# Kernel tuning notes

Measured on AMD Instinct MI355X. Metric: run time of the kernel, lower is better.

The kernel has to match this reference:

```python
import jax, jax.numpy as jnp
import numpy as np

B, P, N = 4, 1024, 16
C1, C2 = 64, 64
K, A = 13, 12  # kernel points (12 s2 dirs + center), rotation anchors
EPS = 1e-12


def _icosahedron_vertices():
    phi = (1.0 + 5.0 ** 0.5) / 2.0
    vs = np.array([
        [-1, phi, 0], [1, phi, 0], [-1, -phi, 0], [1, -phi, 0],
        [0, -1, phi], [0, 1, phi], [0, -1, -phi], [0, 1, -phi],
        [phi, 0, -1], [phi, 0, 1], [-phi, 0, -1], [-phi, 0, 1]], dtype=np.float32)
    return vs


def setup_inputs() -> dict:
    key = jax.random.key(0)
    k1, k2, k3, k4, k5, k6, k7 = jax.random.split(key, 7)
    neighbor_index = jax.random.randint(k1, (B, P, N), 0, P, dtype=jnp.int64) if jax.config.jax_enable_x64 else jax.random.randint(k1, (B, P, N), 0, P, dtype=jnp.int32)
    vertices = jax.random.normal(k2, (B, P, 3), dtype=jnp.float32)
    feature_map = jax.random.normal(k3, (B, C1, P, A), dtype=jnp.float32)
    # xavier-normal init for W (dim_out, dim_in, 36)
    std = (2.0 / (C1 * 36 + C2 * 36)) ** 0.5
    W = jax.random.normal(k4, (C2, C1, 36), dtype=jnp.float32) * std
    vs = jnp.asarray(_icosahedron_vertices())
    # structurally-identical index tables (original precomputed from icosahedral symmetry)
    idx_map = jax.random.randint(k5, (K * A,), 0, 36)  # 156 -> 36 shared weights
    trace_idxv_rot = jax.random.randint(k6, (A, K), 0, K)  # per-anchor kernel permutation
    trace_idxv_rot = trace_idxv_rot.at[:, -1].set(K - 1)  # center maps to itself
    trace_idx_rot = jax.random.randint(k7, (A, A), 0, A)  # per-anchor anchor permutation
    return {"neighbor_index": neighbor_index, "vertices": vertices, "feature_map": feature_map,
            "W": W, "vs": vs, "idx_map": idx_map,
            "trace_idxv_rot": trace_idxv_rot, "trace_idx_rot": trace_idx_rot}


def reference(neighbor_index, vertices, feature_map, W, vs, idx_map, trace_idxv_rot, trace_idx_rot):
    b, p, n = neighbor_index.shape
    c2, c1, _ = W.shape
    # neighbor direction (normalized): [b,p,n,3]
    neighbors = jax.vmap(lambda v, idx: v[idx])(vertices, neighbor_index)
    direction = neighbors - vertices[:, :, None, :]
    dn = direction / jnp.maximum(jnp.linalg.norm(direction, axis=-1, keepdims=True), EPS)
    vs_norm = vs / jnp.maximum(jnp.linalg.norm(vs, axis=1, keepdims=True), EPS)
    # correlation of each neighbor direction with the 12 icosahedron dirs: [b,12,p,n]
    vs_theta = jnp.einsum('bpnc,ac->bapn', dn, vs_norm)
    inter_w = jax.nn.softmax(vs_theta, axis=-1)  # softmax over neighbors
    # gather neighbor features: [b,c1,p,n,a]
    feature_neighbor = jax.vmap(lambda f, idx: f[:, idx, :])(feature_map, neighbor_index)
    # soft-assign neighbors to the 12 kernel directions: [b,c1,12,p,a]
    new_feat = jnp.einsum('bkpn,bcpna->bckpa', inter_w, feature_neighbor)
    # append the center kernel point: [b,c1,13,p,a]
    new_feat = jnp.concatenate([new_feat, feature_map[:, :, None]], axis=2)
    # expand shared weights: [c2,c1,13,12]
    Wmap = W[:, :, idx_map].reshape(c2, c1, K, A)
    # rotated weights per output anchor r: W_eff[c2,c1,r,k,a] = Wmap[c2,c1, kk[r,k], aa[r,a]]
    W_eff = Wmap[:, :, trace_idxv_rot[:, :, None], trace_idx_rot[:, None, :]]
    out = jnp.einsum('bckpa,dcrka->bdpr', new_feat, W_eff)  # [b,c2,p,12]
    return out
```

## Files before the change

kernel.cpp:

```cpp
#include <hip/hip_runtime.h>
#include <hip/hip_bf16.h>
#include <hip/hip_fp16.h>

typedef __attribute__((ext_vector_type(8))) short short8;
typedef __attribute__((ext_vector_type(4))) short s16x4;
typedef __attribute__((ext_vector_type(4))) float f32x4;

#define BN 4
#define PN 1024
#define NN 16
#define C1N 64
#define C2N 64
#define KN 13
#define AN 12
#define KDIM 9984
#define NDIM 768
#define MDIM 4096
#define NSPLIT 5
#define BK 64
#define BM 256
#define BNT 256

__device__ inline unsigned short f2bf(float x){
    unsigned int u = __float_as_uint(x);
    unsigned int r = (u + 0x7fffu + ((u >> 16) & 1u)) >> 16;
    return (unsigned short)r;
}
__device__ inline f32x4 bf4_to_f(s16x4 h){
    f32x4 r;
    r[0] = __uint_as_float(((unsigned)(unsigned short)h[0]) << 16);
    r[1] = __uint_as_float(((unsigned)(unsigned short)h[1]) << 16);
    r[2] = __uint_as_float(((unsigned)(unsigned short)h[2]) << 16);
    r[3] = __uint_as_float(((unsigned)(unsigned short)h[3]) << 16);
    return r;
}

__device__ __forceinline__ void gload16(const unsigned short* g, unsigned short* l){
    __builtin_amdgcn_global_load_lds(
        (const __attribute__((address_space(1))) unsigned int*)(unsigned long long)(uintptr_t)g,
        (__attribute__((address_space(3))) unsigned int*)(unsigned int)(uintptr_t)l,
        16, 0, 0);
}

__global__ __launch_bounds__(256) void k_prep(const int* __restrict__ nbr,
                                              const float* __restrict__ vert,
                                              const float* __restrict__ vs,
                                              const float* __restrict__ W,
                                              const int* __restrict__ idx_map,
                                              const int* __restrict__ tiv,
                                              const int* __restrict__ tir,
                                              const float* __restrict__ fm,
                                              float* __restrict__ iw,
                                              unsigned short* __restrict__ Bm,
                                              unsigned short* __restrict__ Am)
{
    int bid = blockIdx.x;
    if (bid < 192){
        int t = bid * 256 + threadIdx.x;
        int pt = t / AN, a = t - pt * AN;
        int b = pt >> 10;
        float sx = vs[a*3+0], sy = vs[a*3+1], sz = vs[a*3+2];
        float sn = sqrtf(sx*sx + sy*sy + sz*sz);
        float si = 1.0f / fmaxf(sn, 1e-12f);
        sx *= si; sy *= si; sz *= si;
        float vx = vert[pt*3+0], vy = vert[pt*3+1], vz = vert[pt*3+2];
        float tt[NN];
        float mx = -1e30f;
        #pragma unroll
        for (int n = 0; n < NN; n++){
            int g = (b << 10) + nbr[pt*NN + n];
            float dx = vert[g*3+0] - vx;
            float dy = vert[g*3+1] - vy;
            float dz = vert[g*3+2] - vz;
            float nr = sqrtf(dx*dx + dy*dy + dz*dz);
            float inv = 1.0f / fmaxf(nr, 1e-12f);
            tt[n] = (dx*sx + dy*sy + dz*sz) * inv;
            mx = fmaxf(mx, tt[n]);
        }
        float s = 0.0f;
        #pragma unroll
        for (int n = 0; n < NN; n++){ tt[n] = expf(tt[n] - mx); s += tt[n]; }
        float inv = 1.0f / s;
        float* dst = iw + (size_t)t * NN;
        #pragma unroll
        for (int q = 0; q < 4; q++){
            float4 v = make_float4(tt[q*4]*inv, tt[q*4+1]*inv, tt[q*4+2]*inv, tt[q*4+3]*inv);
            *(float4*)(dst + q*4) = v;
        }
    } else if (bid < 2688){
        int t = (bid - 192) * 256 + threadIdx.x;
        int c = t & 63;
        int rest = t >> 6;
        int k = rest % KN;
        int rest2 = rest / KN;
        int r = rest2 % AN;
        int d = rest2 / AN;
        int tv = tiv[r*KN + k];
        const float* wrow = W + (size_t)((d << 6) + c) * 36;
        s16x4 v0, v1, v2;
        #pragma unroll
        for (int a = 0; a < AN; a++){
            int s = idx_map[tv*AN + tir[r*AN + a]];
            unsigned short h = f2bf(wrow[s]);
            if (a < 4) v0[a] = (short)h;
            else if (a < 8) v1[a-4] = (short)h;
            else v2[a-8] = (short)h;
        }
        unsigned short* dst = Bm + ((size_t)(d*AN + r) * KDIM + k*768 + c*AN);
        s16x4* d4 = (s16x4*)dst;
        d4[0] = v0; d4[1] = v1; d4[2] = v2;
    } else {
        int t = (bid - 2688) * 256 + threadIdx.x;
        int a4 = t % 3;
        int rest = t / 3;
        int p = rest & 1023;
        int bc = rest >> 10;
        int c = bc & 63, b = bc >> 6;
        float4 v = *(const float4*)(fm + (size_t)rest * 12 + a4*4);
        s16x4 h;
        h[0] = (short)f2bf(v.x); h[1] = (short)f2bf(v.y);
        h[2] = (short)f2bf(v.z); h[3] = (short)f2bf(v.w);
        int m = (b << 10) + p;
        *(s16x4*)(Am + (size_t)m * KDIM + 9216 + c*12 + a4*4) = h;
    }
}

__global__ __launch_bounds__(256) void k_newfeat(const int* __restrict__ nbr,
                                                 const float* __restrict__ iw,
                                                 unsigned short* Am)
{
    __shared__ int   nbs_s[2][NN];
    __shared__ float iwT_s[2][NN][AN];
    int t = threadIdx.x;
    int w = t >> 6, lane = t & 63;
    int pw = w >> 1, khalf = w & 1;
    int m = blockIdx.x * 2 + pw;
    int b = m >> 10;

    if (khalf == 0){
        if (lane < NN) nbs_s[pw][lane] = nbr[m*NN + lane];
        #pragma unroll
        for (int i = 0; i < 3; i++){
            int idx = lane + i*64;
            int a = idx >> 4, n = idx & 15;
            iwT_s[pw][n][a] = iw[(size_t)m * (AN*NN) + idx];
        }
    }
    __syncthreads();

    f32x4 acc[6][3];
    #pragma unroll
    for (int k = 0; k < 6; k++)
        #pragma unroll
        for (int q = 0; q < 3; q++) acc[k][q] = (f32x4){0.f,0.f,0.f,0.f};

    int kb = khalf * 6;
    const unsigned short* slice = Am + 9216 + (size_t)lane * AN;

    #pragma unroll 2
    for (int n = 0; n < NN; n++){
        int mn = (b << 10) + nbs_s[pw][n];
        const unsigned short* src = slice + (size_t)mn * KDIM;
        s16x4 u0 = *(const s16x4*)(src);
        s16x4 u1 = *(const s16x4*)(src + 4);
        s16x4 u2 = *(const s16x4*)(src + 8);
        f32x4 v0 = bf4_to_f(u0), v1 = bf4_to_f(u1), v2 = bf4_to_f(u2);
        #pragma unroll
        for (int k = 0; k < 6; k++){
            float wv = iwT_s[pw][n][kb + k];
            acc[k][0] += v0 * wv;
            acc[k][1] += v1 * wv;
            acc[k][2] += v2 * wv;
        }
    }

    unsigned short* dst = Am + (size_t)m * KDIM + lane * AN;
    #pragma unroll
    for (int k = 0; k < 6; k++){
        s16x4 h0, h1, h2;
        #pragma unroll
        for (int j = 0; j < 4; j++){
            h0[j] = (short)f2bf(acc[k][0][j]);
            h1[j] = (short)f2bf(acc[k][1][j]);
            h2[j] = (short)f2bf(acc[k][2][j]);
        }
        s16x4* o = (s16x4*)(dst + (kb + k)*768);
        o[0] = h0; o[1] = h1; o[2] = h2;
    }
}

__global__ __launch_bounds__(512, 1) void k_gemm(const unsigned short* __restrict__ Am,
                                                 const unsigned short* __restrict__ Bm,
                                                 __half* __restrict__ part)
{
    __shared__ unsigned short Al[2][BM*BK];
    __shared__ unsigned short Bl[2][BNT*BK];
    int t = threadIdx.x;
    int lane = t & 63, w = t >> 6;
    int wr = w >> 2, wc = w & 3;
    int l15 = lane & 15;
    int kofs = (lane >> 4) * 8;
    int m0 = blockIdx.x * BM, n0 = blockIdx.y * BNT;
    int z = blockIdx.z;
    int kstart = (z == 0) ? 0 : (32 + (z - 1) * 31);
    int nsteps = (z == 0) ? 32 : 31;
    int kbase = kstart * BK;

    const unsigned short* gA[4];
    const unsigned short* gB[4];
    int lofsA[4], lofsB[4];
    #pragma unroll
    for (int i = 0; i < 4; i++){
        int g = i*512 + t;
        int row = g >> 3, ch = g & 7;
        int sch = ch ^ (row & 7);
        gA[i] = Am + (size_t)(m0 + row) * KDIM + kbase + sch*8;
        gB[i] = Bm + (size_t)(n0 + row) * KDIM + kbase + sch*8;
        lofsA[i] = g * 8;
        lofsB[i] = g * 8;
    }

    f32x4 acc[8][4] = {};

#define ISSUE(S,KK) {                                                    \
        _Pragma("unroll")                                                \
        for (int i = 0; i < 4; i++) gload16(gA[i] + (KK), &Al[(S)&1][lofsA[i]]); \
        _Pragma("unroll")                                                \
        for (int i = 0; i < 4; i++) gload16(gB[i] + (KK), &Bl[(S)&1][lofsB[i]]); }

#define BODY(S) { const int cur_ = (S) & 1;                              \
        _Pragma("unroll")                                                \
        for (int kh = 0; kh < 2; kh++){                                  \
            int cc = kh*4 + (kofs >> 3);                                 \
            short8 af[8], bf[4];                                         \
            _Pragma("unroll")                                            \
            for (int i = 0; i < 8; i++){                                 \
                int ra = wr*128 + i*16 + l15;                            \
                af[i] = *(const short8*)&Al[cur_][ra*BK + ((cc ^ (ra & 7)) * 8)]; \
            }                                                            \
            _Pragma("unroll")                                            \
            for (int j = 0; j < 4; j++){                                 \
                int rb = wc*64 + j*16 + l15;                             \
                bf[j] = *(const short8*)&Bl[cur_][rb*BK + ((cc ^ (rb & 7)) * 8)]; \
            }                                                            \
            _Pragma("unroll")                                            \
            for (int i = 0; i < 8; i++){                                 \
                _Pragma("unroll")                                        \
                for (int j = 0; j < 4; j++)                              \
                    acc[i][j] = __builtin_amdgcn_mfma_f32_16x16x32_bf16(af[i], bf[j], acc[i][j], 0, 0, 0); \
            }                                                            \
        } }

    ISSUE(0, 0);

    for (int s = 0; s < nsteps; ++s){
        __builtin_amdgcn_s_barrier();
        if (s + 1 < nsteps){
            ISSUE(s + 1, (s + 1) * BK);
            asm volatile("s_waitcnt vmcnt(8)" ::: "memory");
        } else {
            asm volatile("s_waitcnt vmcnt(0)" ::: "memory");
        }
        __builtin_amdgcn_s_barrier();
        BODY(s);
    }
#undef ISSUE
#undef BODY

    __half* pp = part + (size_t)z * ((size_t)MDIM * NDIM);
    #pragma unroll
    for (int i = 0; i < 8; i++){
        #pragma unroll
        for (int j = 0; j < 4; j++){
            int col = n0 + wc*64 + j*16 + l15;
            #pragma unroll
            for (int q = 0; q < 4; q++){
                int row = m0 + wr*128 + i*16 + (lane >> 4)*4 + q;
                pp[(size_t)row * NDIM + col] = __float2half(acc[i][j][q]);
            }
        }
    }
}

__global__ __launch_bounds__(256) void k_reduce(const __half* __restrict__ part,
                                                float* __restrict__ out)
{
    int t = blockIdx.x * 256 + threadIdx.x;
    if (t >= MDIM * (NDIM/4)) return;
    int m = t / (NDIM/4);
    int n4 = (t - m * (NDIM/4)) * 4;
    f32x4 s = {};
    #pragma unroll
    for (int z = 0; z < NSPLIT; z++){
        const __half2* pz = (const __half2*)(part + (size_t)z * ((size_t)MDIM * NDIM) + (size_t)m * NDIM + n4);
        float2 a = __half22float2(pz[0]);
        float2 b = __half22float2(pz[1]);
        s[0] += a.x; s[1] += a.y; s[2] += b.x; s[3] += b.y;
    }
    int b = m >> 10, p = m & 1023;
    int d = n4 / AN, r = n4 - d*AN;
    *(f32x4*)(out + ((size_t)((b << 6) + d) * PN + p) * AN + r) = s;
}

extern "C" void kernel_launch(void* const* d_in, const int* in_sizes, int n_in,
                              void* d_out, int out_size, void* d_ws, size_t ws_size,
                              hipStream_t stream)
{
    const int*   nbr     = (const int*)  d_in[0];
    const float* vert    = (const float*)d_in[1];
    const float* fm      = (const float*)d_in[2];
    const float* W       = (const float*)d_in[3];
    const float* vs      = (const float*)d_in[4];
    const int*   idx_map = (const int*)  d_in[5];
    const int*   tiv     = (const int*)  d_in[6];
    const int*   tir     = (const int*)  d_in[7];
    float* out = (float*)d_out;

    char* ws = (char*)d_ws;
    float*          iw   = (float*)ws;
    unsigned short* Bm   = (unsigned short*)(ws + 3145728);
    unsigned short* Am   = (unsigned short*)(ws + 18481152);
    __half*         part = (__half*)(ws + 100270080);

    k_prep   <<<5760, 256, 0, stream>>>(nbr, vert, vs, W, idx_map, tiv, tir, fm, iw, Bm, Am);
    k_newfeat<<<MDIM/2, 256, 0, stream>>>(nbr, iw, Am);
    dim3 g(MDIM/BM, NDIM/BNT, NSPLIT);
    k_gemm   <<<g, 512, 0, stream>>>(Am, Bm, part);
    k_reduce <<<(MDIM*(NDIM/4))/256, 256, 0, stream>>>(part, out);
}
```

Measured before the change: 119.2 us.

## Load GEMM B fragments directly from global into registers, bypassing LDS

The B operand tile is no longer staged through shared memory. Each wave now loads its B fragments straight from global memory into double-buffered registers one step ahead, and the wait count is adjusted to cover the extra outstanding loads. This halves LDS usage and removes LDS reads for B. In exchange it adds register pressure and redundant global loads, because the four wave rows each fetch the same B columns. The wait-count accounting with mixed async LDS loads and register loads is also fragile.

Result: slower. 441.2 us (+270.0%).

```diff
diff --git a/kernel.cpp b/kernel.cpp
--- a/kernel.cpp
+++ b/kernel.cpp
@@ -194,7 +194,6 @@
                                                  __half* __restrict__ part)
 {
     __shared__ unsigned short Al[2][BM*BK];
-    __shared__ unsigned short Bl[2][BNT*BK];
     int t = threadIdx.x;
     int lane = t & 63, w = t >> 6;
     int wr = w >> 2, wc = w & 3;
@@ -207,64 +206,72 @@
     int kbase = kstart * BK;
 
     const unsigned short* gA[4];
-    const unsigned short* gB[4];
-    int lofsA[4], lofsB[4];
+    int lofsA[4];
     #pragma unroll
     for (int i = 0; i < 4; i++){
         int g = i*512 + t;
         int row = g >> 3, ch = g & 7;
         int sch = ch ^ (row & 7);
         gA[i] = Am + (size_t)(m0 + row) * KDIM + kbase + sch*8;
-        gB[i] = Bm + (size_t)(n0 + row) * KDIM + kbase + sch*8;
         lofsA[i] = g * 8;
-        lofsB[i] = g * 8;
-    }
+    }
+    const unsigned short* gB0 = Bm + (size_t)(n0 + wc*64 + l15) * KDIM + kbase + kofs;
 
     f32x4 acc[8][4] = {};
-
-#define ISSUE(S,KK) {                                                    \
+    short8 bfA[8], bfB[8];
+
+#define ISSUE(KK) {                                                      \
         _Pragma("unroll")                                                \
-        for (int i = 0; i < 4; i++) gload16(gA[i] + (KK), &Al[(S)&1][lofsA[i]]); \
+        for (int i = 0; i < 4; i++) gload16(gA[i] + (KK), &Al[((KK)/ (BK)) & 1][lofsA[i]]); }
+
+#define ISSUE_S(S,KK) {                                                  \
         _Pragma("unroll")                                                \
-        for (int i = 0; i < 4; i++) gload16(gB[i] + (KK), &Bl[(S)&1][lofsB[i]]); }
-
-#define BODY(S) { const int cur_ = (S) & 1;                              \
+        for (int i = 0; i < 4; i++) gload16(gA[i] + (KK), &Al[(S)&1][lofsA[i]]); }
+
+#define BFLOAD(S,R) {                                                    \
+        _Pragma("unroll")                                                \
+        for (int j = 0; j < 4; j++){                                     \
+            _Pragma("unroll")                                            \
+            for (int kh = 0; kh < 2; kh++){                              \
+                R[j*2+kh] = *(const short8*)(gB0 + (size_t)(j*16)*KDIM + (S)*BK + kh*32); \
+            } } }
+
+#define BODY(S,R) { const int cur_ = (S) & 1;                            \
         _Pragma("unroll")                                                \
         for (int kh = 0; kh < 2; kh++){                                  \
             int cc = kh*4 + (kofs >> 3);                                 \
-            short8 af[8], bf[4];                                         \
+            short8 af[8];                                                \
             _Pragma("unroll")                                            \
             for (int i = 0; i < 8; i++){                                 \
                 int ra = wr*128 + i*16 + l15;                            \
                 af[i] = *(const short8*)&Al[cur_][ra*BK + ((cc ^ (ra & 7)) * 8)]; \
             }                                                            \
             _Pragma("unroll")                                            \
-            for (int j = 0; j < 4; j++){                                 \
-                int rb = wc*64 + j*16 + l15;                             \
-                bf[j] = *(const short8*)&Bl[cur_][rb*BK + ((cc ^ (rb & 7)) * 8)]; \
-            }                                                            \
-            _Pragma("unroll")                                            \
             for (int i = 0; i < 8; i++){                                 \
                 _Pragma("unroll")                                        \
                 for (int j = 0; j < 4; j++)                              \
-                    acc[i][j] = __builtin_amdgcn_mfma_f32_16x16x32_bf16(af[i], bf[j], acc[i][j], 0, 0, 0); \
+                    acc[i][j] = __builtin_amdgcn_mfma_f32_16x16x32_bf16(af[i], R[j*2+kh], acc[i][j], 0, 0, 0); \
             }                                                            \
         } }
 
-    ISSUE(0, 0);
+    ISSUE_S(0, 0);
+    BFLOAD(0, bfA);
 
     for (int s = 0; s < nsteps; ++s){
         __builtin_amdgcn_s_barrier();
         if (s + 1 < nsteps){
-            ISSUE(s + 1, (s + 1) * BK);
-            asm volatile("s_waitcnt vmcnt(8)" ::: "memory");
+            ISSUE_S(s + 1, (s + 1) * BK);
+            if ((s + 1) & 1) { BFLOAD(s + 1, bfB); } else { BFLOAD(s + 1, bfA); }
+            asm volatile("s_waitcnt vmcnt(12)" ::: "memory");
         } else {
             asm volatile("s_waitcnt vmcnt(0)" ::: "memory");
         }
         __builtin_amdgcn_s_barrier();
-        BODY(s);
+        if (s & 1) { BODY(s, bfB); } else { BODY(s, bfA); }
     }
 #undef ISSUE
+#undef ISSUE_S
+#undef BFLOAD
 #undef BODY
 
     __half* pp = part + (size_t)z * ((size_t)MDIM * NDIM);
```

## Restructure GEMM mainloop into fine-grained 8-phase ping-pong pipeline with split LDS halves

Applied to the files above, without the earlier changes.

Rewrites the k_gemm main loop so that each K step is split into four sub-phases over half-tiles of A and B. Global-to-LDS loads for the next steps are interleaved between MFMA clusters, and s_setprio raises MFMA priority inside each cluster. The LDS layout changes to two 32-wide K halves with a new XOR swizzle. The split-K partitioning also changes from 32/31 steps to an even 32-step split with a shorter last slice. The goal is to hide memory latency behind MFMA work, at the cost of more barriers and more delicate vmcnt accounting.

Result: no change. 121.5 us (+1.9%).

```diff
diff --git a/kernel.cpp b/kernel.cpp
--- a/kernel.cpp
+++ b/kernel.cpp
@@ -193,79 +193,105 @@
                                                  const unsigned short* __restrict__ Bm,
                                                  __half* __restrict__ part)
 {
-    __shared__ unsigned short Al[2][BM*BK];
-    __shared__ unsigned short Bl[2][BNT*BK];
+    __shared__ unsigned short Al[2][2*256*32];
+    __shared__ unsigned short Bl[2][2*256*32];
     int t = threadIdx.x;
     int lane = t & 63, w = t >> 6;
     int wr = w >> 2, wc = w & 3;
     int l15 = lane & 15;
-    int kofs = (lane >> 4) * 8;
+    int lq  = lane >> 4;
     int m0 = blockIdx.x * BM, n0 = blockIdx.y * BNT;
     int z = blockIdx.z;
-    int kstart = (z == 0) ? 0 : (32 + (z - 1) * 31);
-    int nsteps = (z == 0) ? 32 : 31;
-    int kbase = kstart * BK;
-
-    const unsigned short* gA[4];
-    const unsigned short* gB[4];
-    int lofsA[4], lofsB[4];
-    #pragma unroll
-    for (int i = 0; i < 4; i++){
-        int g = i*512 + t;
-        int row = g >> 3, ch = g & 7;
-        int sch = ch ^ (row & 7);
-        gA[i] = Am + (size_t)(m0 + row) * KDIM + kbase + sch*8;
-        gB[i] = Bm + (size_t)(n0 + row) * KDIM + kbase + sch*8;
-        lofsA[i] = g * 8;
-        lofsB[i] = g * 8;
-    }
+    int kbase = z * 32 * BK;
+    int nsteps = (z == 4) ? 28 : 32;
+
+    int rA  = (t >> 8) * 128 + ((t >> 2) & 63);
+    int chA = t & 3;
+    int csA = chA ^ ((rA >> 1) & 3);
+    int rB0 = t >> 2,          chB0 = t & 3;
+    int rB1 = (512 + t) >> 2,  chB1 = (512 + t) & 3;
+    int csB0 = chB0 ^ ((rB0 >> 1) & 3);
+    int csB1 = chB1 ^ ((rB1 >> 1) & 3);
+
+    const unsigned short* gAq0 = Am + (size_t)(m0 + rA)      * KDIM + kbase + csA*8;
+    const unsigned short* gAq1 = Am + (size_t)(m0 + 64 + rA) * KDIM + kbase + csA*8;
+    const unsigned short* gBp0 = Bm + (size_t)(n0 + rB0) * KDIM + kbase + csB0*8;
+    const unsigned short* gBp1 = Bm + (size_t)(n0 + rB1) * KDIM + kbase + csB1*8;
+    int ldsAq0 = rA*32 + chA*8;
+    int ldsAq1 = (64 + rA)*32 + chA*8;
+    int ldsB0  = rB0*32 + chB0*8;
+    int ldsB1  = rB1*32 + chB1*8;
 
     f32x4 acc[8][4] = {};
 
-#define ISSUE(S,KK) {                                                    \
-        _Pragma("unroll")                                                \
-        for (int i = 0; i < 4; i++) gload16(gA[i] + (KK), &Al[(S)&1][lofsA[i]]); \
-        _Pragma("unroll")                                                \
-        for (int i = 0; i < 4; i++) gload16(gB[i] + (KK), &Bl[(S)&1][lofsB[i]]); }
-
-#define BODY(S) { const int cur_ = (S) & 1;                              \
-        _Pragma("unroll")                                                \
-        for (int kh = 0; kh < 2; kh++){                                  \
-            int cc = kh*4 + (kofs >> 3);                                 \
-            short8 af[8], bf[4];                                         \
-            _Pragma("unroll")                                            \
-            for (int i = 0; i < 8; i++){                                 \
-                int ra = wr*128 + i*16 + l15;                            \
-                af[i] = *(const short8*)&Al[cur_][ra*BK + ((cc ^ (ra & 7)) * 8)]; \
-            }                                                            \
-            _Pragma("unroll")                                            \
-            for (int j = 0; j < 4; j++){                                 \
-                int rb = wc*64 + j*16 + l15;                             \
-                bf[j] = *(const short8*)&Bl[cur_][rb*BK + ((cc ^ (rb & 7)) * 8)]; \
-            }                                                            \
-            _Pragma("unroll")                                            \
-            for (int i = 0; i < 8; i++){                                 \
-                _Pragma("unroll")                                        \
-                for (int j = 0; j < 4; j++)                              \
-                    acc[i][j] = __builtin_amdgcn_mfma_f32_16x16x32_bf16(af[i], bf[j], acc[i][j], 0, 0, 0); \
-            }                                                            \
-        } }
-
-    ISSUE(0, 0);
-
-    for (int s = 0; s < nsteps; ++s){
-        __builtin_amdgcn_s_barrier();
-        if (s + 1 < nsteps){
-            ISSUE(s + 1, (s + 1) * BK);
-            asm volatile("s_waitcnt vmcnt(8)" ::: "memory");
-        } else {
-            asm volatile("s_waitcnt vmcnt(0)" ::: "memory");
-        }
-        __builtin_amdgcn_s_barrier();
-        BODY(s);
-    }
-#undef ISSUE
-#undef BODY
+#define SA(U,Q,KH,BUF) gload16(((Q)? gAq1 : gAq0) + (U)*64 + (KH)*32, \
+                               &Al[BUF][(KH)*8192 + ((Q)? ldsAq1 : ldsAq0)])
+#define SB(U,KH,BUF) { gload16(gBp0 + (U)*64 + (KH)*32, &Bl[BUF][(KH)*8192 + ldsB0]); \
+                       gload16(gBp1 + (U)*64 + (KH)*32, &Bl[BUF][(KH)*8192 + ldsB1]); }
+
+#define RAF(i,Q,KH,CUR) ({ int ra_ = wr*128 + (Q)*64 + (i)*16 + l15; \
+        *(const short8*)&Al[CUR][(KH)*8192 + ra_*32 + ((lq ^ ((ra_>>1)&3))*8)]; })
+#define RBF(j,KH,CUR) ({ int rb_ = wc*64 + (j)*16 + l15; \
+        *(const short8*)&Bl[CUR][(KH)*8192 + rb_*32 + ((lq ^ ((rb_>>1)&3))*8)]; })
+
+#define MF(A,B,C) __builtin_amdgcn_mfma_f32_16x16x32_bf16(A,B,C,0,0,0)
+#define MM16(QO) { \
+    acc[QO+0][0]=MF(a0,bq0,acc[QO+0][0]); acc[QO+0][1]=MF(a0,bq1,acc[QO+0][1]); acc[QO+0][2]=MF(a0,bq2,acc[QO+0][2]); acc[QO+0][3]=MF(a0,bq3,acc[QO+0][3]); \
+    acc[QO+1][0]=MF(a1,bq0,acc[QO+1][0]); acc[QO+1][1]=MF(a1,bq1,acc[QO+1][1]); acc[QO+1][2]=MF(a1,bq2,acc[QO+1][2]); acc[QO+1][3]=MF(a1,bq3,acc[QO+1][3]); \
+    acc[QO+2][0]=MF(a2,bq0,acc[QO+2][0]); acc[QO+2][1]=MF(a2,bq1,acc[QO+2][1]); acc[QO+2][2]=MF(a2,bq2,acc[QO+2][2]); acc[QO+2][3]=MF(a2,bq3,acc[QO+2][3]); \
+    acc[QO+3][0]=MF(a3,bq0,acc[QO+3][0]); acc[QO+3][1]=MF(a3,bq1,acc[QO+3][1]); acc[QO+3][2]=MF(a3,bq2,acc[QO+3][2]); acc[QO+3][3]=MF(a3,bq3,acc[QO+3][3]); }
+
+#define BAR()  __builtin_amdgcn_s_barrier()
+#define LGKM0() asm volatile("s_waitcnt lgkmcnt(0)" ::: "memory")
+
+    SA(0,0,0,0); SA(0,1,0,0); SA(0,0,1,0); SA(0,1,1,0); SB(0,0,0); SB(0,1,0);
+    SA(1,0,0,1); SA(1,1,0,1); SA(1,0,1,1); SB(1,0,1); SB(1,1,1);
+    asm volatile("s_waitcnt vmcnt(7)" ::: "memory");
+    BAR();
+
+    for (int u = 0; u < nsteps; ++u){
+        const int cur = u & 1;
+        const int nxt = cur ^ 1;
+        const bool s1 = (u + 1 < nsteps);
+        const bool s2 = (u + 2 < nsteps);
+        short8 a0,a1,a2,a3, bq0,bq1,bq2,bq3;
+
+        a0=RAF(0,0,0,cur); a1=RAF(1,0,0,cur); a2=RAF(2,0,0,cur); a3=RAF(3,0,0,cur);
+        bq0=RBF(0,0,cur);  bq1=RBF(1,0,cur);  bq2=RBF(2,0,cur);  bq3=RBF(3,0,cur);
+        if (s1) SA(u+1, 1, 1, nxt);
+        BAR(); LGKM0();
+        __builtin_amdgcn_s_setprio(1); MM16(0); __builtin_amdgcn_s_setprio(0);
+        BAR();
+
+        a0=RAF(0,1,0,cur); a1=RAF(1,1,0,cur); a2=RAF(2,1,0,cur); a3=RAF(3,1,0,cur);
+        if (s2){ SA(u+2,0,0,cur); SB(u+2,0,cur); }
+        BAR(); LGKM0();
+        __builtin_amdgcn_s_setprio(1); MM16(4); __builtin_amdgcn_s_setprio(0);
+        BAR();
+
+        a0=RAF(0,0,1,cur); a1=RAF(1,0,1,cur); a2=RAF(2,0,1,cur); a3=RAF(3,0,1,cur);
+        bq0=RBF(0,1,cur);  bq1=RBF(1,1,cur);  bq2=RBF(2,1,cur);  bq3=RBF(3,1,cur);
+        if (s2) SA(u+2,1,0,cur);
+        BAR(); LGKM0();
+        __builtin_amdgcn_s_setprio(1); MM16(0); __builtin_amdgcn_s_setprio(0);
+        BAR();
+
+        a0=RAF(0,1,1,cur); a1=RAF(1,1,1,cur); a2=RAF(2,1,1,cur); a3=RAF(3,1,1,cur);
+        if (s2){ SA(u+2,0,1,cur); SB(u+2,1,cur); }
+        BAR(); LGKM0();
+        __builtin_amdgcn_s_setprio(1); MM16(4); __builtin_amdgcn_s_setprio(0);
+        if (s2) { asm volatile("s_waitcnt vmcnt(7)" ::: "memory"); }
+        else    { asm volatile("s_waitcnt vmcnt(0)" ::: "memory"); }
+        BAR();
+    }
+#undef SA
+#undef SB
+#undef RAF
+#undef RBF
+#undef MF
+#undef MM16
+#undef BAR
+#undef LGKM0
 
     __half* pp = part + (size_t)z * ((size_t)MDIM * NDIM);
     #pragma unroll
```
